# Kernel tuning notes

Hardware: AMD Instinct MI355X
Metric: run time of the kernel (lower is better)

Reference implementation:

```python
import jax, jax.numpy as jnp
import numpy as np

DIM_MODEL = 1024
DIM_K = 64
DIM_V = 64
H = 16
B = 2
S = 2048


def setup_inputs() -> dict:
    key = jax.random.key(0)
    ks = jax.random.split(key, 11)
    s = 0.02
    return {
        "Q": jax.random.normal(ks[0], (B, S, DIM_MODEL), jnp.float32),
        "K": jax.random.normal(ks[1], (B, S, DIM_MODEL), jnp.float32),
        "V": jax.random.normal(ks[2], (B, S, DIM_MODEL), jnp.float32),
        "Wq": jax.random.normal(ks[3], (DIM_MODEL, H * DIM_K), jnp.float32) * s,
        "bq": jnp.zeros((H * DIM_K,), jnp.float32),
        "Wk": jax.random.normal(ks[4], (DIM_MODEL, H * DIM_K), jnp.float32) * s,
        "bk": jnp.zeros((H * DIM_K,), jnp.float32),
        "Wv": jax.random.normal(ks[5], (DIM_MODEL, H * DIM_V), jnp.float32) * s,
        "bv": jnp.zeros((H * DIM_V,), jnp.float32),
        "Wo": jax.random.normal(ks[6], (H * DIM_V, DIM_MODEL), jnp.float32) * s,
        "bo": jnp.zeros((DIM_MODEL,), jnp.float32),
    }


def reference(Q, K, V, Wq, bq, Wk, bk, Wv, bv, Wo, bo):
    b, len_q = Q.shape[0], Q.shape[1]
    # QKV projections, split heads: [b, h, S, d]
    q = (Q @ Wq + bq).reshape(b, len_q, H, DIM_K).transpose(0, 2, 1, 3)
    k = (K @ Wk + bk).reshape(b, K.shape[1], H, DIM_K).transpose(0, 2, 1, 3)
    v = (V @ Wv + bv).reshape(b, V.shape[1], H, DIM_V).transpose(0, 2, 1, 3)
    # FAITHFUL QUIRK: original scales by sqrt(K.shape[0]) == batch size, not dim_k
    scale = 1.0 / np.sqrt(b).astype(np.float32)
    att = jnp.einsum('bhqd,bhkd->bhqk', q * scale, k)
    att = jax.nn.softmax(att, axis=-1)
    out = jnp.einsum('bhqk,bhkd->bhqd', att, v)  # [b,h,S,dv]
    out = out.transpose(0, 2, 1, 3).reshape(b, len_q, H * DIM_V)
    return out @ Wo + bo
```

## Files before the change

### kernel.cpp

```cpp
#include <hip/hip_runtime.h>
#include <hip/hip_bf16.h>


using bf16 = __hip_bfloat16;
typedef __attribute__((ext_vector_type(4))) float f32x4;
typedef __attribute__((ext_vector_type(8))) short bf16x8;

__device__ __forceinline__ void gload_lds16(const void* gsrc, void* ldst) {
    __builtin_amdgcn_global_load_lds(
        (const __attribute__((address_space(1))) void*)gsrc,
        (__attribute__((address_space(3))) void*)ldst,
        16, 0, 0);
}

__device__ __forceinline__ float fexp2(float x) {
    float r; asm("v_exp_f32 %0, %1" : "=v"(r) : "v"(x)); return r;
}

__device__ __forceinline__ unsigned cvtpk(float a, float b) {
    unsigned d; asm("v_cvt_pk_bf16_f32 %0, %1, %2" : "=v"(d) : "v"(a), "v"(b));
    return d;
}

__device__ __forceinline__ void pls32(unsigned &a, unsigned &b) {
    asm("v_permlane32_swap_b32 %0, %1" : "+v"(a), "+v"(b));
}
__device__ __forceinline__ void pls16(unsigned &a, unsigned &b) {
    asm("v_permlane16_swap_b32 %0, %1" : "+v"(a), "+v"(b));
}

__device__ __forceinline__ unsigned pack2bf(float a, float b) {
    unsigned short ua = __builtin_bit_cast(unsigned short, __float2bfloat16(a));
    unsigned short ub = __builtin_bit_cast(unsigned short, __float2bfloat16(b));
    return (unsigned)ua | ((unsigned)ub << 16);
}

__global__ void prep_kernel(const float* __restrict__ X0, const float* __restrict__ X1,
                            const float* __restrict__ X2,
                            bf16* __restrict__ O0, bf16* __restrict__ O1, bf16* __restrict__ O2,
                            const float* __restrict__ W0, const float* __restrict__ W1,
                            const float* __restrict__ W2, const float* __restrict__ W3,
                            bf16* __restrict__ T0, bf16* __restrict__ T1,
                            bf16* __restrict__ T2, bf16* __restrict__ T3,
                            int n4) {
    const int z = blockIdx.z;
    if (z < 3) {
        const float* in = z == 0 ? X0 : (z == 1 ? X1 : X2);
        bf16* out = z == 0 ? O0 : (z == 1 ? O1 : O2);
        int idx = blockIdx.x * blockDim.x + threadIdx.x;
        int stride = gridDim.x * blockDim.x;
        for (int i = idx; i < n4; i += stride) {
            float4 v = reinterpret_cast<const float4*>(in)[i];
            reinterpret_cast<uint2*>(out)[i] = make_uint2(pack2bf(v.x, v.y), pack2bf(v.z, v.w));
        }
    } else {
        const int w = z - 3;
        const float* W = w == 0 ? W0 : (w == 1 ? W1 : (w == 2 ? W2 : W3));
        bf16* WT = w == 0 ? T0 : (w == 1 ? T1 : (w == 2 ? T2 : T3));
        __shared__ float t[32][33];
        int bx = (blockIdx.x & 31) * 32, by = (blockIdx.x >> 5) * 32;
        int x = threadIdx.x & 31, y = threadIdx.x >> 5;
        #pragma unroll
        for (int i = 0; i < 4; ++i)
            t[y + 8*i][x] = W[(size_t)(by + y + 8*i) * 1024 + bx + x];
        __syncthreads();
        #pragma unroll
        for (int i = 0; i < 4; ++i)
            WT[(size_t)(bx + y + 8*i) * 1024 + by + x] = __float2bfloat16(t[x][y + 8*i]);
    }
}

template<int NTILE>
__global__ __launch_bounds__(256, 3)
void gemm_bt(const bf16* __restrict__ A0, const bf16* __restrict__ A1, const bf16* __restrict__ A2,
             const bf16* __restrict__ B0, const bf16* __restrict__ B1, const bf16* __restrict__ B2,
             const float* __restrict__ bi0, const float* __restrict__ bi1, const float* __restrict__ bi2,
             void* __restrict__ O0, void* __restrict__ O1, void* __restrict__ O2,
             int mode_base)
{
    const int f = blockIdx.x;
    int x, y, z;
    if (NTILE == 128) {
        const int s = f >> 3;
        y = s & 7;
        const int t = (f & 7) + 8 * (s >> 3);
        x = t & 31; z = t >> 5;
    } else {
        const int s = f >> 3;
        y = s & 15;
        x = (f & 7) + 8 * (s >> 4);
        z = 0;
    }
    const bf16* A  = z == 0 ? A0 : (z == 1 ? A1 : A2);
    const bf16* BT = z == 0 ? B0 : (z == 1 ? B1 : B2);
    const float* bias = z == 0 ? bi0 : (z == 1 ? bi1 : bi2);
    void* Cout = z == 0 ? O0 : (z == 1 ? O1 : O2);
    const int mode = mode_base + z;

    __shared__ __align__(16) char Sbuf[16384 + NTILE * 128];
    char* Abuf = Sbuf;
    char* Bbuf = Sbuf + 16384;
    constexpr int MF = (NTILE == 128) ? 4 : 2;
    const int tid = threadIdx.x;
    const int wave = tid >> 6, lane = tid & 63;
    const int g = lane >> 4, ln = lane & 15;
    const int m0 = x * 128, n0 = y * NTILE;
    const int wm = (NTILE == 128) ? (wave >> 1) * 64 : wave * 32;
    const int wn = (NTILE == 128) ? (wave & 1) * 64 : 0;
    const int lnsw = (ln & 7) << 4;

    f32x4 acc[MF][4] = {};

    for (int k0 = 0; k0 < 1024; k0 += 64) {
        __syncthreads();
        #pragma unroll
        for (int rd = 0; rd < 4; ++rd) {
            int row = rd * 32 + (tid >> 3);
            int src = ((tid & 7) * 16) ^ (((tid >> 3) & 7) << 4);
            gload_lds16((const char*)(A + (size_t)(m0 + row) * 1024 + k0) + src,
                        Abuf + rd * 4096 + tid * 16);
        }
        #pragma unroll
        for (int rd = 0; rd < NTILE / 32; ++rd) {
            int row = rd * 32 + (tid >> 3);
            int src = ((tid & 7) * 16) ^ (((tid >> 3) & 7) << 4);
            gload_lds16((const char*)(BT + (size_t)(n0 + row) * 1024 + k0) + src,
                        Bbuf + rd * 4096 + tid * 16);
        }
        __syncthreads();
        #pragma unroll
        for (int kk = 0; kk < 2; ++kk) {
            bf16x8 af[MF], bfr[4];
            #pragma unroll
            for (int mf = 0; mf < MF; ++mf)
                af[mf] = *(const bf16x8*)&Abuf[(wm + mf*16 + ln) * 128 + ((kk*64 + g*16) ^ lnsw)];
            #pragma unroll
            for (int nf = 0; nf < 4; ++nf)
                bfr[nf] = *(const bf16x8*)&Bbuf[(wn + nf*16 + ln) * 128 + ((kk*64 + g*16) ^ lnsw)];
            #pragma unroll
            for (int mf = 0; mf < MF; ++mf)
                #pragma unroll
                for (int nf = 0; nf < 4; ++nf)
                    acc[mf][nf] = __builtin_amdgcn_mfma_f32_16x16x32_bf16(af[mf], bfr[nf], acc[mf][nf], 0, 0, 0);
        }
    }

    const float scl = (mode == 0) ? (0.70710678118654752f * 1.44269504088896340f) : 1.0f;

    if (mode == 2) {
        #pragma unroll
        for (int mf = 0; mf < MF; ++mf) {
            #pragma unroll
            for (int nf = 0; nf < 4; ++nf) {
                int col = n0 + wn + nf*16 + ln;
                float bv = bias[col];
                int row0 = m0 + wm + mf*16 + g*4;
                int b = row0 >> 11, ss = row0 & 2047;
                int hh = col >> 6, dv = col & 63;
                bf16* dst = (bf16*)Cout + (((size_t)(b*16 + hh) * 64 + dv) << 11) + ss;
                *(uint2*)dst = make_uint2(
                    pack2bf(acc[mf][nf][0] + bv, acc[mf][nf][1] + bv),
                    pack2bf(acc[mf][nf][2] + bv, acc[mf][nf][3] + bv));
            }
        }
    } else if (mode == 0 || mode == 1) {
        __syncthreads();
        #pragma unroll
        for (int mf = 0; mf < MF; ++mf) {
            #pragma unroll
            for (int nf = 0; nf < 4; ++nf) {
                int tcol = wn + nf*16 + ln;
                float bv = bias[n0 + tcol];
                #pragma unroll
                for (int r = 0; r < 4; ++r) {
                    int trow = wm + mf*16 + g*4 + r;
                    *(unsigned short*)(Sbuf + trow * (NTILE*2) + tcol * 2) =
                        __builtin_bit_cast(unsigned short,
                            __float2bfloat16((acc[mf][nf][r] + bv) * scl));
                }
            }
        }
        __syncthreads();
        constexpr int TPR = NTILE / 8;
        const int rr = tid / TPR, cc = (tid % TPR) * 8;
        #pragma unroll
        for (int it = 0; it < 128 / (256 / TPR); ++it) {
            int row = it * (256 / TPR) + rr;
            uint4 v = *(const uint4*)(Sbuf + row * (NTILE*2) + cc * 2);
            *(uint4*)((bf16*)Cout + (size_t)(m0 + row) * 1024 + n0 + cc) = v;
        }
    } else {
        #pragma unroll
        for (int p = 0; p < 2; ++p) {
            __syncthreads();
            #pragma unroll
            for (int mf = 0; mf < MF; ++mf) {
                #pragma unroll
                for (int j = 0; j < 2; ++j) {
                    int nf = p * 2 + j;
                    int tcol = j*16 + ln;
                    float bv = bias[n0 + wn + nf*16 + ln];
                    #pragma unroll
                    for (int r = 0; r < 4; ++r) {
                        int trow = wm + mf*16 + g*4 + r;
                        *(float*)(Sbuf + trow * 128 + tcol * 4) = acc[mf][nf][r] + bv;
                    }
                }
            }
            __syncthreads();
            const int rr = tid >> 3, cc = (tid & 7) * 4;
            #pragma unroll
            for (int it = 0; it < 4; ++it) {
                int row = it * 32 + rr;
                uint4 v = *(const uint4*)(Sbuf + row * 128 + cc * 4);
                *(uint4*)((float*)Cout + (size_t)(m0 + row) * 1024 + n0 + p*32 + cc) = v;
            }
        }
    }
}

__global__ __launch_bounds__(256, 2)
void attn_kernel(const bf16* __restrict__ qh, const bf16* __restrict__ kh,
                 const bf16* __restrict__ vt, bf16* __restrict__ aout)
{
    __shared__ __align__(16) bf16 Kls[2][128 * 64];
    __shared__ __align__(16) bf16 Vls[2][64 * 128];
    const int f = blockIdx.x;
    const int xcd = f & 7, s = f >> 3, i = s & 15, ghi = s >> 4;
    const int bh = xcd + 8 * ghi;
    const int b = bh >> 4, h = bh & 15;
    const int q0 = i * 128;

    const int tid = threadIdx.x;
    const int wave = tid >> 6, lane = tid & 63;
    const int g = lane >> 4, ln = lane & 15;
    const int srow = lane >> 3;
    const int scol = ((lane & 7) * 16) ^ ((srow & 7) << 4);
    const int lnsw = (ln & 7) << 4;

    const bf16* kbase = kh + (size_t)(b * 2048) * 1024 + h * 64;
    const bf16* vbase = vt + (size_t)bh * 64 * 2048;

    const int vrow_in = lane >> 4;
    const int vcol16 = lane & 15;

    bf16x8 qf[2][2];
    #pragma unroll
    for (int nf = 0; nf < 2; ++nf) {
        const bf16* qrow = qh + (size_t)(b*2048 + q0 + wave*32 + nf*16 + ln) * 1024 + h*64;
        qf[nf][0] = *(const bf16x8*)(qrow + g*8);
        qf[nf][1] = *(const bf16x8*)(qrow + 32 + g*8);
    }

    auto stageKV = [&](int kv0, int buf) {
        #pragma unroll
        for (int c2 = 0; c2 < 4; ++c2) {
            int c = wave * 4 + c2;
            int krow = c * 8 + srow;
            gload_lds16((const char*)(kbase + (size_t)(kv0 + krow) * 1024) + scol,
                        (char*)&Kls[buf][0] + c * 1024);
        }
        #pragma unroll
        for (int c2 = 0; c2 < 4; ++c2) {
            int c = wave * 4 + c2;
            int vrow = c * 4 + vrow_in;
            int sc16 = vcol16 ^ (vrow & 15);
            gload_lds16((const char*)(vbase + (size_t)vrow * 2048 + kv0) + sc16 * 16,
                        (char*)&Vls[buf][0] + c * 1024);
        }
    };

    stageKV(0, 0);

    f32x4 oacc[4][2] = {};
    f32x4 lacc[2] = {};
    union PU { unsigned u[4]; bf16x8 v; };
    PU ones;
    ones.u[0] = ones.u[1] = ones.u[2] = ones.u[3] = 0x3F803F80u;

    for (int t = 0; t < 16; ++t) {
        const int cur = t & 1;
        if (t < 15) {
            stageKV((t + 1) * 128, cur ^ 1);
            asm volatile("s_waitcnt vmcnt(8)\n\ts_barrier" ::: "memory");
        } else {
            asm volatile("s_waitcnt vmcnt(0)\n\ts_barrier" ::: "memory");
        }
        __builtin_amdgcn_sched_barrier(0);

        const char* Kc = (const char*)&Kls[cur][0];
        const char* Vc = (const char*)&Vls[cur][0];

        f32x4 sacA[4][2] = {}, sacB[4][2] = {};
        __builtin_amdgcn_s_setprio(1);
        #pragma unroll
        for (int kk = 0; kk < 2; ++kk) {
            bf16x8 kf[4];
            #pragma unroll
            for (int mf = 0; mf < 4; ++mf)
                kf[mf] = *(const bf16x8*)(Kc + (mf*16 + ln) * 128 + ((kk*64 + g*16) ^ lnsw));
            #pragma unroll
            for (int mf = 0; mf < 4; ++mf)
                #pragma unroll
                for (int nf = 0; nf < 2; ++nf)
                    sacA[mf][nf] = __builtin_amdgcn_mfma_f32_16x16x32_bf16(kf[mf], qf[nf][kk], sacA[mf][nf], 0, 0, 0);
        }
        #pragma unroll
        for (int kk = 0; kk < 2; ++kk) {
            bf16x8 kf[4];
            #pragma unroll
            for (int mf = 0; mf < 4; ++mf)
                kf[mf] = *(const bf16x8*)(Kc + (64 + mf*16 + ln) * 128 + ((kk*64 + g*16) ^ lnsw));
            #pragma unroll
            for (int mf = 0; mf < 4; ++mf)
                #pragma unroll
                for (int nf = 0; nf < 2; ++nf)
                    sacB[mf][nf] = __builtin_amdgcn_mfma_f32_16x16x32_bf16(kf[mf], qf[nf][kk], sacB[mf][nf], 0, 0, 0);
        }
        __builtin_amdgcn_s_setprio(0);

        PU pfh[2][2][2];
        #pragma unroll
        for (int ha = 0; ha < 2; ++ha) {
            f32x4 (&sac)[4][2] = ha ? sacB : sacA;
            #pragma unroll
            for (int nf = 0; nf < 2; ++nf) {
                unsigned w[4][2];
                #pragma unroll
                for (int mf = 0; mf < 4; ++mf) {
                    float e0 = fexp2(sac[mf][nf][0]);
                    float e1 = fexp2(sac[mf][nf][1]);
                    float e2 = fexp2(sac[mf][nf][2]);
                    float e3 = fexp2(sac[mf][nf][3]);
                    w[mf][0] = cvtpk(e0, e1);
                    w[mf][1] = cvtpk(e2, e3);
                }
                #pragma unroll
                for (int kk = 0; kk < 2; ++kk) {
                    #pragma unroll
                    for (int rp = 0; rp < 2; ++rp) {
                        unsigned a = w[2*kk][rp], bb = w[2*kk + 1][rp];
                        pls32(a, bb);
                        pls16(a, bb);
                        pfh[ha][nf][kk].u[rp] = a;
                        pfh[ha][nf][kk].u[2 + rp] = bb;
                    }
                }
            }
        }

        __builtin_amdgcn_s_setprio(1);
        #pragma unroll
        for (int ha = 0; ha < 2; ++ha) {
            #pragma unroll
            for (int kk = 0; kk < 2; ++kk) {
                bf16x8 vf[4];
                #pragma unroll
                for (int mf = 0; mf < 4; ++mf)
                    vf[mf] = *(const bf16x8*)(Vc + (mf*16 + ln) * 256 + (((ha*8 + kk*4 + g) ^ ln) << 4));
                #pragma unroll
                for (int nf = 0; nf < 2; ++nf)
                    lacc[nf] = __builtin_amdgcn_mfma_f32_16x16x32_bf16(ones.v, pfh[ha][nf][kk].v, lacc[nf], 0, 0, 0);
                #pragma unroll
                for (int mf = 0; mf < 4; ++mf)
                    #pragma unroll
                    for (int nf = 0; nf < 2; ++nf)
                        oacc[mf][nf] = __builtin_amdgcn_mfma_f32_16x16x32_bf16(vf[mf], pfh[ha][nf][kk].v, oacc[mf][nf], 0, 0, 0);
            }
        }
        __builtin_amdgcn_s_setprio(0);
        __builtin_amdgcn_sched_barrier(0);
        asm volatile("s_barrier" ::: "memory");
    }

    #pragma unroll
    for (int nf = 0; nf < 2; ++nf) {
        float inv = 1.0f / lacc[nf][0];
        int q = q0 + wave*32 + nf*16 + ln;
        bf16* orow = aout + (size_t)(b*2048 + q) * 1024 + h * 64;
        #pragma unroll
        for (int mf = 0; mf < 4; ++mf) {
            *(uint2*)(orow + mf*16 + g*4) = make_uint2(
                pack2bf(oacc[mf][nf][0] * inv, oacc[mf][nf][1] * inv),
                pack2bf(oacc[mf][nf][2] * inv, oacc[mf][nf][3] * inv));
        }
    }
}

extern "C" void kernel_launch(void* const* d_in, const int* in_sizes, int n_in,
                              void* d_out, int out_size, void* d_ws, size_t ws_size,
                              hipStream_t stream)
{
    const float* Q  = (const float*)d_in[0];
    const float* K  = (const float*)d_in[1];
    const float* V  = (const float*)d_in[2];
    const float* Wq = (const float*)d_in[3];
    const float* bq = (const float*)d_in[4];
    const float* Wk = (const float*)d_in[5];
    const float* bk = (const float*)d_in[6];
    const float* Wv = (const float*)d_in[7];
    const float* bv = (const float*)d_in[8];
    const float* Wo = (const float*)d_in[9];
    const float* bo = (const float*)d_in[10];

    char* ws = (char*)d_ws;
    const size_t MB = 1024 * 1024;
    bf16* Qbf  = (bf16*)(ws + 0);
    bf16* Kbf  = (bf16*)(ws + 8*MB);
    bf16* Vbf  = (bf16*)(ws + 16*MB);
    bf16* WqT  = (bf16*)(ws + 24*MB);
    bf16* WkT  = (bf16*)(ws + 26*MB);
    bf16* WvT  = (bf16*)(ws + 28*MB);
    bf16* WoT  = (bf16*)(ws + 30*MB);
    bf16* qhp  = (bf16*)(ws + 32*MB);
    bf16* khp  = (bf16*)(ws + 40*MB);
    bf16* vtp  = (bf16*)(ws + 48*MB);
    bf16* aout = (bf16*)(ws + 0);

    const int n4 = (2 * 2048 * 1024) / 4;
    prep_kernel<<<dim3(1024, 1, 7), 256, 0, stream>>>(Q, K, V, Qbf, Kbf, Vbf,
                                                      Wq, Wk, Wv, Wo, WqT, WkT, WvT, WoT, n4);

    gemm_bt<128><<<768, 256, 0, stream>>>(Qbf, Kbf, Vbf, WqT, WkT, WvT,
                                          bq, bk, bv, qhp, khp, vtp, 0);

    attn_kernel<<<512, 256, 0, stream>>>(qhp, khp, vtp, aout);

    gemm_bt<64><<<512, 256, 0, stream>>>(aout, aout, aout, WoT, WoT, WoT,
                                         bo, bo, bo, d_out, d_out, d_out, 3);
}
```

Baseline: 106.0 us.

## Double-buffer GEMM LDS tiles to overlap global loads with MFMA

Splits the projection GEMM's shared-memory staging into two buffers so that the tiles for the next k-step are loaded while the current step's MFMAs run. Waits use explicit vmcnt counts and raw s_barrier in place of __syncthreads. LDS per block doubles, and the 128-tile variant's launch bound drops to 2 blocks per SM. That lowers occupancy, and the manual waitcnt accounting is fragile.

```diff
diff --git a/kernel.cpp b/kernel.cpp
--- a/kernel.cpp
+++ b/kernel.cpp
@@ -71,7 +71,7 @@
 }
 
 template<int NTILE>
-__global__ __launch_bounds__(256, 3)
+__global__ __launch_bounds__(256, (NTILE == 128) ? 2 : 3)
 void gemm_bt(const bf16* __restrict__ A0, const bf16* __restrict__ A1, const bf16* __restrict__ A2,
              const bf16* __restrict__ B0, const bf16* __restrict__ B1, const bf16* __restrict__ B2,
              const float* __restrict__ bi0, const float* __restrict__ bi1, const float* __restrict__ bi2,
@@ -97,9 +97,10 @@
     void* Cout = z == 0 ? O0 : (z == 1 ? O1 : O2);
     const int mode = mode_base + z;
 
-    __shared__ __align__(16) char Sbuf[16384 + NTILE * 128];
-    char* Abuf = Sbuf;
-    char* Bbuf = Sbuf + 16384;
+    constexpr int ABYTES = 16384;
+    constexpr int BBYTES = NTILE * 128;
+    constexpr int BUFB   = ABYTES + BBYTES;
+    __shared__ __align__(16) char Sbuf[2 * BUFB];
     constexpr int MF = (NTILE == 128) ? 4 : 2;
     const int tid = threadIdx.x;
     const int wave = tid >> 6, lane = tid & 63;
@@ -109,40 +110,58 @@
     const int wn = (NTILE == 128) ? (wave & 1) * 64 : 0;
     const int lnsw = (ln & 7) << 4;
 
-    f32x4 acc[MF][4] = {};
-
-    for (int k0 = 0; k0 < 1024; k0 += 64) {
-        __syncthreads();
+    auto stage = [&](int k0, int buf) {
+        char* Ab = Sbuf + buf * BUFB;
+        char* Bb = Ab + ABYTES;
         #pragma unroll
         for (int rd = 0; rd < 4; ++rd) {
             int row = rd * 32 + (tid >> 3);
             int src = ((tid & 7) * 16) ^ (((tid >> 3) & 7) << 4);
             gload_lds16((const char*)(A + (size_t)(m0 + row) * 1024 + k0) + src,
-                        Abuf + rd * 4096 + tid * 16);
+                        Ab + rd * 4096 + tid * 16);
         }
         #pragma unroll
         for (int rd = 0; rd < NTILE / 32; ++rd) {
             int row = rd * 32 + (tid >> 3);
             int src = ((tid & 7) * 16) ^ (((tid >> 3) & 7) << 4);
             gload_lds16((const char*)(BT + (size_t)(n0 + row) * 1024 + k0) + src,
-                        Bbuf + rd * 4096 + tid * 16);
-        }
-        __syncthreads();
+                        Bb + rd * 4096 + tid * 16);
+        }
+    };
+
+    f32x4 acc[MF][4] = {};
+    stage(0, 0);
+
+    for (int k = 0; k < 16; ++k) {
+        const int cur = k & 1;
+        if (k < 15) {
+            stage((k + 1) * 64, cur ^ 1);
+            if (NTILE == 128) asm volatile("s_waitcnt vmcnt(8)\n\ts_barrier" ::: "memory");
+            else              asm volatile("s_waitcnt vmcnt(6)\n\ts_barrier" ::: "memory");
+        } else {
+            asm volatile("s_waitcnt vmcnt(0)\n\ts_barrier" ::: "memory");
+        }
+        __builtin_amdgcn_sched_barrier(0);
+
+        const char* Ab = Sbuf + cur * BUFB;
+        const char* Bb = Ab + ABYTES;
         #pragma unroll
         for (int kk = 0; kk < 2; ++kk) {
             bf16x8 af[MF], bfr[4];
             #pragma unroll
             for (int mf = 0; mf < MF; ++mf)
-                af[mf] = *(const bf16x8*)&Abuf[(wm + mf*16 + ln) * 128 + ((kk*64 + g*16) ^ lnsw)];
+                af[mf] = *(const bf16x8*)(Ab + (wm + mf*16 + ln) * 128 + ((kk*64 + g*16) ^ lnsw));
             #pragma unroll
             for (int nf = 0; nf < 4; ++nf)
-                bfr[nf] = *(const bf16x8*)&Bbuf[(wn + nf*16 + ln) * 128 + ((kk*64 + g*16) ^ lnsw)];
+                bfr[nf] = *(const bf16x8*)(Bb + (wn + nf*16 + ln) * 128 + ((kk*64 + g*16) ^ lnsw));
             #pragma unroll
             for (int mf = 0; mf < MF; ++mf)
                 #pragma unroll
                 for (int nf = 0; nf < 4; ++nf)
                     acc[mf][nf] = __builtin_amdgcn_mfma_f32_16x16x32_bf16(af[mf], bfr[nf], acc[mf][nf], 0, 0, 0);
         }
+        __builtin_amdgcn_sched_barrier(0);
+        asm volatile("s_barrier" ::: "memory");
     }
 
     const float scl = (mode == 0) ? (0.70710678118654752f * 1.44269504088896340f) : 1.0f;
```

Measured after the change: 105.0 us. Within noise of the previous version (-0.9%).
